# Optimization experiments

Hardware: AMD Instinct MI355X
Metric: run time of the kernel (lower is better)

Reference implementation:

```python
import jax, jax.numpy as jnp
import numpy as np

N, D, V = 4096, 1024, 50257


def setup_inputs() -> dict:
    key = jax.random.key(0)
    kx, kw, kt = jax.random.split(key, 3)
    x = jax.random.normal(kx, (N, D), dtype=jnp.float32)
    weight = jax.random.normal(kw, (V, D), dtype=jnp.float32) * 0.02
    target = jax.random.randint(kt, (N,), 0, V, dtype=jnp.int64)
    return {"x": x, "weight": weight, "target": target}


def reference(x, weight, target):
    # fused fc -> log_softmax -> nll_loss (mean reduction)
    logits = jnp.einsum("nd,vd->nv", x, weight)          # [N, V]
    logp = jax.nn.log_softmax(logits, axis=-1)            # stable log-softmax
    nll = -jnp.take_along_axis(logp, target[:, None].astype(jnp.int32), axis=-1)[:, 0]
    return jnp.mean(nll)
```

## Files before the change

kernel.cpp:

```cpp
#include <hip/hip_runtime.h>
#include <hip/hip_bf16.h>
#include <stdint.h>

#define NROWS 4096
#define DDIM  1024
#define VDIM  50257
#define VPAD  50304

#define PITCH   80
#define B_BASE  20480
#define STAGE   30720
typedef __bf16 bf16;
typedef __bf16 bf16x4 __attribute__((ext_vector_type(4)));
typedef __bf16 bf16x8 __attribute__((ext_vector_type(8)));
typedef float  f32x16 __attribute__((ext_vector_type(16)));

__global__ __launch_bounds__(256)
void cvt_kernel(const float* __restrict__ src, bf16* __restrict__ dst, size_t n_src) {
  size_t i = ((size_t)blockIdx.x * 256 + threadIdx.x) * 8;
  float4 f0 = make_float4(0.f, 0.f, 0.f, 0.f), f1 = f0;
  if (i < n_src) { f0 = *(const float4*)(src + i); f1 = *(const float4*)(src + i + 4); }
  bf16x8 o = { (__bf16)f0.x, (__bf16)f0.y, (__bf16)f0.z, (__bf16)f0.w,
               (__bf16)f1.x, (__bf16)f1.y, (__bf16)f1.z, (__bf16)f1.w };
  *(bf16x8*)(dst + i) = o;
}

__global__ __launch_bounds__(256)
void tlogit_kernel(const float* __restrict__ x, const float* __restrict__ w,
                   const int* __restrict__ tgt, float* __restrict__ lt) {
  int n = blockIdx.x;
  int t = tgt[n];
  const float4* xr = (const float4*)(x + (size_t)n * DDIM);
  const float4* wr = (const float4*)(w + (size_t)t * DDIM);
  float4 a = xr[threadIdx.x];
  float4 b = wr[threadIdx.x];
  float s = a.x * b.x + a.y * b.y + a.z * b.z + a.w * b.w;
  #pragma unroll
  for (int m = 32; m; m >>= 1) s += __shfl_down(s, m);
  __shared__ float red[4];
  if ((threadIdx.x & 63) == 0) red[threadIdx.x >> 6] = s;
  __syncthreads();
  if (threadIdx.x == 0) lt[n] = red[0] + red[1] + red[2] + red[3];
}

__global__ __launch_bounds__(256, 2)
void gemm_lse_kernel(const bf16* __restrict__ xb,
                     const bf16* __restrict__ wb,
                     float* __restrict__ S) {
  __shared__ __align__(16) unsigned char smem[2 * STAGE];

  const int tid  = threadIdx.x;
  const int wid  = tid >> 6;
  const int lane = tid & 63;
  const int c31  = lane & 31;
  const int h    = lane >> 5;

  const int m0 = blockIdx.x * 256;
  const int v0 = blockIdx.y * 128;
  const int wave_m = wid >> 1;
  const int wave_n = wid & 1;

  const int lr = lane >> 2;
  const int lc = lane & 3;
  const bf16* gA[4]; uint32_t wAo[4];
  #pragma unroll
  for (int a = 0; a < 4; ++a) {
    int r = (wid * 4 + a) * 16 + lr;
    gA[a]  = xb + (size_t)(m0 + r) * DDIM + lc * 8;
    wAo[a] = (uint32_t)(r * PITCH + lc * 16);
  }
  const bf16* gB[2]; uint32_t wBo[2];
  #pragma unroll
  for (int b = 0; b < 2; ++b) {
    int r = (wid * 2 + b) * 16 + lr;
    gB[b]  = wb + (size_t)(v0 + r) * DDIM + lc * 8;
    wBo[b] = (uint32_t)(B_BASE + r * PITCH + lc * 16);
  }

  uint32_t aoff[4][2], boff[2][2];
  #pragma unroll
  for (int mi = 0; mi < 4; ++mi)
    #pragma unroll
    for (int kk = 0; kk < 2; ++kk)
      aoff[mi][kk] = (uint32_t)((wave_m * 128 + mi * 32 + c31) * PITCH + (kk * 2 + h) * 16);
  #pragma unroll
  for (int ni = 0; ni < 2; ++ni)
    #pragma unroll
    for (int kk = 0; kk < 2; ++kk)
      boff[ni][kk] = (uint32_t)(B_BASE + (wave_n * 64 + ni * 32 + c31) * PITCH + (kk * 2 + h) * 16);

  f32x16 acc[4][2] = {};
  bf16x8 rA[4], rB[2];

  #pragma unroll
  for (int a = 0; a < 4; ++a) rA[a] = *(const bf16x8*)gA[a];
  #pragma unroll
  for (int b = 0; b < 2; ++b) rB[b] = *(const bf16x8*)gB[b];
  #pragma unroll
  for (int a = 0; a < 4; ++a) *(bf16x8*)(smem + wAo[a]) = rA[a];
  #pragma unroll
  for (int b = 0; b < 2; ++b) *(bf16x8*)(smem + wBo[b]) = rB[b];
  #pragma unroll
  for (int a = 0; a < 4; ++a) rA[a] = *(const bf16x8*)(gA[a] + 32);
  #pragma unroll
  for (int b = 0; b < 2; ++b) rB[b] = *(const bf16x8*)(gB[b] + 32);
  __syncthreads();

  #pragma unroll 2
  for (int k = 0; k < 32; ++k) {
    const uint32_t sb = (uint32_t)(k & 1) * STAGE;
    const uint32_t nb = STAGE - sb;
    #pragma unroll
    for (int kk = 0; kk < 2; ++kk) {
      bf16x8 af[4], bfv[2];
      #pragma unroll
      for (int mi = 0; mi < 4; ++mi) af[mi]  = *(const bf16x8*)(smem + sb + aoff[mi][kk]);
      #pragma unroll
      for (int ni = 0; ni < 2; ++ni) bfv[ni] = *(const bf16x8*)(smem + sb + boff[ni][kk]);
      if (kk == 0) {
        __builtin_amdgcn_sched_barrier(0);
        if (k + 1 < 32) {
          #pragma unroll
          for (int a = 0; a < 4; ++a) *(bf16x8*)(smem + nb + wAo[a]) = rA[a];
          #pragma unroll
          for (int b = 0; b < 2; ++b) *(bf16x8*)(smem + nb + wBo[b]) = rB[b];
        }
        if (k + 2 < 32) {
          #pragma unroll
          for (int a = 0; a < 4; ++a) rA[a] = *(const bf16x8*)(gA[a] + (k + 2) * 32);
          #pragma unroll
          for (int b = 0; b < 2; ++b) rB[b] = *(const bf16x8*)(gB[b] + (k + 2) * 32);
        }
        __builtin_amdgcn_sched_barrier(0);
      }
      #pragma unroll
      for (int mi = 0; mi < 4; ++mi)
        #pragma unroll
        for (int ni = 0; ni < 2; ++ni)
          acc[mi][ni] = __builtin_amdgcn_mfma_f32_32x32x16_bf16(
              af[mi], bfv[ni], acc[mi][ni], 0, 0, 0);
    }
    __syncthreads();
  }

  #pragma unroll
  for (int mi = 0; mi < 4; ++mi) {
    #pragma unroll
    for (int r = 0; r < 16; ++r) {
      float pacc = 0.f;
      #pragma unroll
      for (int ni = 0; ni < 2; ++ni) {
        int v = v0 + wave_n * 64 + ni * 32 + c31;
        float e = __expf(acc[mi][ni][r]);
        pacc += (v < VDIM) ? e : 0.f;
      }
      pacc += __shfl_xor(pacc, 16);
      pacc += __shfl_xor(pacc, 8);
      pacc += __shfl_xor(pacc, 4);
      pacc += __shfl_xor(pacc, 2);
      pacc += __shfl_xor(pacc, 1);
      if (c31 == 0) {
        int row = m0 + wave_m * 128 + mi * 32 + (r & 3) + 8 * (r >> 2) + 4 * h;
        atomicAdd(&S[row], pacc);
      }
    }
  }
}

__global__ __launch_bounds__(1024)
void loss_kernel(const float* __restrict__ S, const float* __restrict__ lt,
                 float* __restrict__ out) {
  float s = 0.f;
  for (int n = threadIdx.x; n < NROWS; n += 1024)
    s += logf(S[n]) - lt[n];
  #pragma unroll
  for (int m = 32; m; m >>= 1) s += __shfl_down(s, m);
  __shared__ float red[16];
  if ((threadIdx.x & 63) == 0) red[threadIdx.x >> 6] = s;
  __syncthreads();
  if (threadIdx.x == 0) {
    float t = 0.f;
    #pragma unroll
    for (int i = 0; i < 16; ++i) t += red[i];
    out[0] = t / (float)NROWS;
  }
}

extern "C" void kernel_launch(void* const* d_in, const int* in_sizes, int n_in,
                              void* d_out, int out_size, void* d_ws, size_t ws_size,
                              hipStream_t stream) {
  const float* x = (const float*)d_in[0];
  const float* w = (const float*)d_in[1];
  const int*   t = (const int*)d_in[2];
  float* out = (float*)d_out;

  char* ws = (char*)d_ws;
  const size_t wb_bytes = (size_t)VPAD * DDIM * sizeof(bf16);
  const size_t xb_bytes = (size_t)NROWS * DDIM * sizeof(bf16);
  bf16*  wb = (bf16*)ws;
  bf16*  xb = (bf16*)(ws + wb_bytes);
  float* S  = (float*)(ws + wb_bytes + xb_bytes);
  float* lt = S + NROWS;

  if (ws_size < wb_bytes + xb_bytes + 2 * NROWS * sizeof(float)) return;

  hipMemsetAsync(S, 0, NROWS * sizeof(float), stream);
  cvt_kernel<<<(VPAD * (DDIM / 8)) / 256, 256, 0, stream>>>(w, wb, (size_t)VDIM * DDIM);
  cvt_kernel<<<(NROWS * (DDIM / 8)) / 256, 256, 0, stream>>>(x, xb, (size_t)NROWS * DDIM);
  tlogit_kernel<<<NROWS, 256, 0, stream>>>(x, w, t, lt);

  dim3 grid(NROWS / 256, VPAD / 128);
  gemm_lse_kernel<<<grid, 256, 0, stream>>>(xb, wb, S);

  loss_kernel<<<1, 1024, 0, stream>>>(S, lt, out);
}
```

Before: 815.2 us.

## Quantize GEMM operands to FP8 with scaling and swizzle block order

Converts x and weight to scaled FP8 (scales 8 and 64) instead of bf16, and runs the logits GEMM with fp8 MFMA instructions, descaling before the exp. This halves operand bytes and doubles MFMA throughput per instruction, reducing conversion and GEMM cost. It also remaps block indices so groups of vocab tiles are traversed together for better L2 reuse. The risk is accuracy loss from FP8 precision in the logsumexp.

Result: no change. 802.3 us (-1.6%).

```diff
diff --git a/kernel.cpp b/kernel.cpp
--- a/kernel.cpp
+++ b/kernel.cpp
@@ -6,23 +6,36 @@
 #define DDIM  1024
 #define VDIM  50257
 #define VPAD  50304
-
-#define PITCH   80
-#define B_BASE  20480
-#define STAGE   30720
-typedef __bf16 bf16;
-typedef __bf16 bf16x4 __attribute__((ext_vector_type(4)));
-typedef __bf16 bf16x8 __attribute__((ext_vector_type(8)));
-typedef float  f32x16 __attribute__((ext_vector_type(16)));
+#define NVT   393
+#define NMT   16
+
+#define DESCALE (1.0f / 512.0f)
+
+#define PITCH  80
+#define B_BASE 20480
+#define STAGE  30720
+
+typedef long  i64;
+typedef i64   i64x2 __attribute__((ext_vector_type(2)));
+typedef float f32x16 __attribute__((ext_vector_type(16)));
 
 __global__ __launch_bounds__(256)
-void cvt_kernel(const float* __restrict__ src, bf16* __restrict__ dst, size_t n_src) {
-  size_t i = ((size_t)blockIdx.x * 256 + threadIdx.x) * 8;
-  float4 f0 = make_float4(0.f, 0.f, 0.f, 0.f), f1 = f0;
-  if (i < n_src) { f0 = *(const float4*)(src + i); f1 = *(const float4*)(src + i + 4); }
-  bf16x8 o = { (__bf16)f0.x, (__bf16)f0.y, (__bf16)f0.z, (__bf16)f0.w,
-               (__bf16)f1.x, (__bf16)f1.y, (__bf16)f1.z, (__bf16)f1.w };
-  *(bf16x8*)(dst + i) = o;
+void cvtq_kernel(const float* __restrict__ src, uint32_t* __restrict__ dst,
+                 size_t n_src, float scale) {
+  size_t i = ((size_t)blockIdx.x * 256 + threadIdx.x) * 16;
+  uint32_t o[4] = {0u, 0u, 0u, 0u};
+  if (i < n_src) {
+    const float4* s = (const float4*)(src + i);
+    #pragma unroll
+    for (int d = 0; d < 4; ++d) {
+      float4 f = s[d];
+      uint32_t v = 0;
+      v = __builtin_amdgcn_cvt_pk_fp8_f32(f.x * scale, f.y * scale, v, false);
+      v = __builtin_amdgcn_cvt_pk_fp8_f32(f.z * scale, f.w * scale, v, true);
+      o[d] = v;
+    }
+  }
+  *(uint4*)(dst + i / 4) = make_uint4(o[0], o[1], o[2], o[3]);
 }
 
 __global__ __launch_bounds__(256)
@@ -44,8 +57,8 @@
 }
 
 __global__ __launch_bounds__(256, 2)
-void gemm_lse_kernel(const bf16* __restrict__ xb,
-                     const bf16* __restrict__ wb,
+void gemm_lse_kernel(const uint8_t* __restrict__ xq,
+                     const uint8_t* __restrict__ wq,
                      float* __restrict__ S) {
   __shared__ __align__(16) unsigned char smem[2 * STAGE];
 
@@ -55,91 +68,121 @@
   const int c31  = lane & 31;
   const int h    = lane >> 5;
 
-  const int m0 = blockIdx.x * 256;
-  const int v0 = blockIdx.y * 128;
+  const int flat = blockIdx.x + blockIdx.y * 16;
+  int bm, vt;
+  if (flat >= (NVT - 1) * 16) { vt = NVT - 1; bm = flat - (NVT - 1) * 16; }
+  else { vt = (flat >> 7) * 8 + (flat & 7); bm = (flat >> 3) & 15; }
+  const int m0 = bm * 256;
+  const int v0 = vt * 128;
+
   const int wave_m = wid >> 1;
   const int wave_n = wid & 1;
 
   const int lr = lane >> 2;
   const int lc = lane & 3;
-  const bf16* gA[4]; uint32_t wAo[4];
+  const uint8_t* gA[4]; uint32_t wAo[4];
   #pragma unroll
   for (int a = 0; a < 4; ++a) {
     int r = (wid * 4 + a) * 16 + lr;
-    gA[a]  = xb + (size_t)(m0 + r) * DDIM + lc * 8;
-    wAo[a] = (uint32_t)(r * PITCH + lc * 16);
-  }
-  const bf16* gB[2]; uint32_t wBo[2];
+    gA[a]  = xq + (size_t)(m0 + r) * DDIM + lc * 16;
+    wAo[a] = (uint32_t)(r * PITCH + lc * 8);
+  }
+  const uint8_t* gB[2]; uint32_t wBo[2];
   #pragma unroll
   for (int b = 0; b < 2; ++b) {
     int r = (wid * 2 + b) * 16 + lr;
-    gB[b]  = wb + (size_t)(v0 + r) * DDIM + lc * 8;
-    wBo[b] = (uint32_t)(B_BASE + r * PITCH + lc * 16);
+    gB[b]  = wq + (size_t)(v0 + r) * DDIM + lc * 16;
+    wBo[b] = (uint32_t)(B_BASE + r * PITCH + lc * 8);
   }
 
   uint32_t aoff[4][2], boff[2][2];
   #pragma unroll
   for (int mi = 0; mi < 4; ++mi)
     #pragma unroll
-    for (int kk = 0; kk < 2; ++kk)
-      aoff[mi][kk] = (uint32_t)((wave_m * 128 + mi * 32 + c31) * PITCH + (kk * 2 + h) * 16);
+    for (int j = 0; j < 2; ++j)
+      aoff[mi][j] = (uint32_t)((wave_m * 128 + mi * 32 + c31) * PITCH + h * 32 + j * 16);
   #pragma unroll
   for (int ni = 0; ni < 2; ++ni)
     #pragma unroll
-    for (int kk = 0; kk < 2; ++kk)
-      boff[ni][kk] = (uint32_t)(B_BASE + (wave_n * 64 + ni * 32 + c31) * PITCH + (kk * 2 + h) * 16);
+    for (int j = 0; j < 2; ++j)
+      boff[ni][j] = (uint32_t)(B_BASE + (wave_n * 64 + ni * 32 + c31) * PITCH + h * 32 + j * 16);
 
   f32x16 acc[4][2] = {};
-  bf16x8 rA[4], rB[2];
-
-  #pragma unroll
-  for (int a = 0; a < 4; ++a) rA[a] = *(const bf16x8*)gA[a];
-  #pragma unroll
-  for (int b = 0; b < 2; ++b) rB[b] = *(const bf16x8*)gB[b];
-  #pragma unroll
-  for (int a = 0; a < 4; ++a) *(bf16x8*)(smem + wAo[a]) = rA[a];
-  #pragma unroll
-  for (int b = 0; b < 2; ++b) *(bf16x8*)(smem + wBo[b]) = rB[b];
-  #pragma unroll
-  for (int a = 0; a < 4; ++a) rA[a] = *(const bf16x8*)(gA[a] + 32);
-  #pragma unroll
-  for (int b = 0; b < 2; ++b) rB[b] = *(const bf16x8*)(gB[b] + 32);
+  i64x2 rA[4], rB[2];
+
+  #pragma unroll
+  for (int a = 0; a < 4; ++a) rA[a] = *(const i64x2*)gA[a];
+  #pragma unroll
+  for (int b = 0; b < 2; ++b) rB[b] = *(const i64x2*)gB[b];
+  #pragma unroll
+  for (int a = 0; a < 4; ++a) {
+    *(i64*)(smem + wAo[a])      = rA[a].x;
+    *(i64*)(smem + wAo[a] + 32) = rA[a].y;
+  }
+  #pragma unroll
+  for (int b = 0; b < 2; ++b) {
+    *(i64*)(smem + wBo[b])      = rB[b].x;
+    *(i64*)(smem + wBo[b] + 32) = rB[b].y;
+  }
+  #pragma unroll
+  for (int a = 0; a < 4; ++a) rA[a] = *(const i64x2*)(gA[a] + 64);
+  #pragma unroll
+  for (int b = 0; b < 2; ++b) rB[b] = *(const i64x2*)(gB[b] + 64);
   __syncthreads();
 
   #pragma unroll 2
-  for (int k = 0; k < 32; ++k) {
+  for (int k = 0; k < 16; ++k) {
     const uint32_t sb = (uint32_t)(k & 1) * STAGE;
     const uint32_t nb = STAGE - sb;
-    #pragma unroll
-    for (int kk = 0; kk < 2; ++kk) {
-      bf16x8 af[4], bfv[2];
-      #pragma unroll
-      for (int mi = 0; mi < 4; ++mi) af[mi]  = *(const bf16x8*)(smem + sb + aoff[mi][kk]);
-      #pragma unroll
-      for (int ni = 0; ni < 2; ++ni) bfv[ni] = *(const bf16x8*)(smem + sb + boff[ni][kk]);
-      if (kk == 0) {
-        __builtin_amdgcn_sched_barrier(0);
-        if (k + 1 < 32) {
+
+    i64x2 af[4][2], bf[2][2];
+    #pragma unroll
+    for (int mi = 0; mi < 4; ++mi)
+      #pragma unroll
+      for (int j = 0; j < 2; ++j)
+        af[mi][j] = *(const i64x2*)(smem + sb + aoff[mi][j]);
+    #pragma unroll
+    for (int ni = 0; ni < 2; ++ni)
+      #pragma unroll
+      for (int j = 0; j < 2; ++j)
+        bf[ni][j] = *(const i64x2*)(smem + sb + boff[ni][j]);
+
+    __builtin_amdgcn_sched_barrier(0);
+
+    if (k + 1 < 16) {
+      #pragma unroll
+      for (int a = 0; a < 4; ++a) {
+        *(i64*)(smem + nb + wAo[a])      = rA[a].x;
+        *(i64*)(smem + nb + wAo[a] + 32) = rA[a].y;
+      }
+      #pragma unroll
+      for (int b = 0; b < 2; ++b) {
+        *(i64*)(smem + nb + wBo[b])      = rB[b].x;
+        *(i64*)(smem + nb + wBo[b] + 32) = rB[b].y;
+      }
+    }
+    if (k + 2 < 16) {
+      #pragma unroll
+      for (int a = 0; a < 4; ++a) rA[a] = *(const i64x2*)(gA[a] + (k + 2) * 64);
+      #pragma unroll
+      for (int b = 0; b < 2; ++b) rB[b] = *(const i64x2*)(gB[b] + (k + 2) * 64);
+    }
+
+    __builtin_amdgcn_sched_barrier(0);
+
+    #pragma unroll
+    for (int j = 0; j < 2; ++j)
+      #pragma unroll
+      for (int tt = 0; tt < 2; ++tt)
+        #pragma unroll
+        for (int mi = 0; mi < 4; ++mi)
           #pragma unroll
-          for (int a = 0; a < 4; ++a) *(bf16x8*)(smem + nb + wAo[a]) = rA[a];
-          #pragma unroll
-          for (int b = 0; b < 2; ++b) *(bf16x8*)(smem + nb + wBo[b]) = rB[b];
-        }
-        if (k + 2 < 32) {
-          #pragma unroll
-          for (int a = 0; a < 4; ++a) rA[a] = *(const bf16x8*)(gA[a] + (k + 2) * 32);
-          #pragma unroll
-          for (int b = 0; b < 2; ++b) rB[b] = *(const bf16x8*)(gB[b] + (k + 2) * 32);
-        }
-        __builtin_amdgcn_sched_barrier(0);
-      }
-      #pragma unroll
-      for (int mi = 0; mi < 4; ++mi)
-        #pragma unroll
-        for (int ni = 0; ni < 2; ++ni)
-          acc[mi][ni] = __builtin_amdgcn_mfma_f32_32x32x16_bf16(
-              af[mi], bfv[ni], acc[mi][ni], 0, 0, 0);
-    }
+          for (int ni = 0; ni < 2; ++ni)
+            acc[mi][ni] = __builtin_amdgcn_mfma_f32_32x32x16_fp8_fp8(
+                tt ? af[mi][j].y : af[mi][j].x,
+                tt ? bf[ni][j].y : bf[ni][j].x,
+                acc[mi][ni], 0, 0, 0);
+
     __syncthreads();
   }
 
@@ -151,7 +194,7 @@
       #pragma unroll
       for (int ni = 0; ni < 2; ++ni) {
         int v = v0 + wave_n * 64 + ni * 32 + c31;
-        float e = __expf(acc[mi][ni][r]);
+        float e = __expf(acc[mi][ni][r] * DESCALE);
         pacc += (v < VDIM) ? e : 0.f;
       }
       pacc += __shfl_xor(pacc, 16);
@@ -195,22 +238,24 @@
   float* out = (float*)d_out;
 
   char* ws = (char*)d_ws;
-  const size_t wb_bytes = (size_t)VPAD * DDIM * sizeof(bf16);
-  const size_t xb_bytes = (size_t)NROWS * DDIM * sizeof(bf16);
-  bf16*  wb = (bf16*)ws;
-  bf16*  xb = (bf16*)(ws + wb_bytes);
-  float* S  = (float*)(ws + wb_bytes + xb_bytes);
-  float* lt = S + NROWS;
-
-  if (ws_size < wb_bytes + xb_bytes + 2 * NROWS * sizeof(float)) return;
+  const size_t wq_bytes = (size_t)VPAD * DDIM;
+  const size_t xq_bytes = (size_t)NROWS * DDIM;
+  uint8_t* wq = (uint8_t*)ws;
+  uint8_t* xq = (uint8_t*)(ws + wq_bytes);
+  float*   S  = (float*)(ws + wq_bytes + xq_bytes);
+  float*   lt = S + NROWS;
+
+  if (ws_size < wq_bytes + xq_bytes + 2 * NROWS * sizeof(float)) return;
 
   hipMemsetAsync(S, 0, NROWS * sizeof(float), stream);
-  cvt_kernel<<<(VPAD * (DDIM / 8)) / 256, 256, 0, stream>>>(w, wb, (size_t)VDIM * DDIM);
-  cvt_kernel<<<(NROWS * (DDIM / 8)) / 256, 256, 0, stream>>>(x, xb, (size_t)NROWS * DDIM);
+  cvtq_kernel<<<VPAD / 4, 256, 0, stream>>>(w, (uint32_t*)wq,
+                                            (size_t)VDIM * DDIM, 64.0f);
+  cvtq_kernel<<<NROWS / 4, 256, 0, stream>>>(x, (uint32_t*)xq,
+                                             (size_t)NROWS * DDIM, 8.0f);
   tlogit_kernel<<<NROWS, 256, 0, stream>>>(x, w, t, lt);
 
-  dim3 grid(NROWS / 256, VPAD / 128);
-  gemm_lse_kernel<<<grid, 256, 0, stream>>>(xb, wb, S);
+  dim3 grid(NMT, NVT);
+  gemm_lse_kernel<<<grid, 256, 0, stream>>>(xq, wq, S);
 
   loss_kernel<<<1, 1024, 0, stream>>>(S, lt, out);
 }
```
